# Optimization experiments

Hardware: AMD Instinct MI355X
Metric: run time of the kernel (lower is better)

## Reference

```python
import jax, jax.numpy as jnp
import numpy as np

N, E, D, LM, NF, M = 512, 16384, 1280, 1024, 256, 64

def setup_inputs() -> dict:
    key = jax.random.key(0)
    ks = jax.random.split(key, 10)
    lm_embedding = jax.random.normal(ks[0], (1, N + 2, LM), jnp.float32)
    node_feat = jax.random.normal(ks[1], (N, NF), jnp.float32)
    edge_feat = jax.random.uniform(ks[2], (E, 1), jnp.float32)
    src = jax.random.randint(ks[3], (E,), 0, N)
    dst = jax.random.randint(ks[4], (E,), 0, N)
    mask_index = jax.random.randint(ks[5], (M,), 0, N)
    W_g = jax.random.normal(ks[6], (D, D), jnp.float32) / np.sqrt(D).astype(np.float32)
    b_g = jnp.zeros((D,), jnp.float32)
    W_d = jax.random.normal(ks[7], (D, 1), jnp.float32) / np.sqrt(D).astype(np.float32)
    b_d = jnp.zeros((1,), jnp.float32)
    W_m = jax.random.normal(ks[8], (D, 2), jnp.float32) / np.sqrt(D).astype(np.float32)
    b_m = jnp.zeros((2,), jnp.float32)
    return {"lm_embedding": lm_embedding, "node_feat": node_feat, "edge_feat": edge_feat,
            "src": src, "dst": dst, "mask_index": mask_index,
            "W_g": W_g, "b_g": b_g, "W_d": W_d, "b_d": b_d, "W_m": W_m, "b_m": b_m}

def reference(lm_embedding, node_feat, edge_feat, src, dst, mask_index,
              W_g, b_g, W_d, b_d, W_m, b_m):
    # concat LM embedding (strip BOS/EOS) with structural features -> (N, D)
    h = jnp.concatenate([lm_embedding[0, 1:-1, :], node_feat], axis=1)
    # GINConv('max'): messages = h[src] * edge_weight, max-reduce onto dst
    msg = h[src] * edge_feat                                   # (E, D)
    neigh = jax.ops.segment_max(msg, dst, num_segments=h.shape[0])
    neigh = jnp.where(jnp.isneginf(neigh), 0.0, neigh)         # isolated nodes -> 0 (DGL semantics)
    rst = (h + neigh) @ W_g + b_g                              # (1+eps)*h + neigh, eps=0, then Linear
    node_output = rst + h                                      # residual
    # dis_pred[i, j] = sigmoid(W_d . (h_j - h_i) + b_d); collapse to per-node projection
    p = (node_output @ W_d)[:, 0]                              # (N,)
    dis_pred = jax.nn.sigmoid(p[None, :] - p[:, None] + b_d[0])[..., None]  # (N, N, 1)
    mask_pred = jnp.tanh(node_output[mask_index] @ W_m + b_m)  # (M, 2)
    return (dis_pred, mask_pred)
```

## Files before the change

### kernel.cpp

```cpp
#include <hip/hip_runtime.h>
#include <float.h>
#include <math.h>

#define N 512
#define E 16384
#define D 1280
#define LMDIM 1024
#define NFDIM 256
#define M 64
#define MAXDEG 512

__device__ __forceinline__ float4 h_vec4(const float* __restrict__ lm,
                                         const float* __restrict__ nf,
                                         int i, int t) {
  return (t < 256) ? *(const float4*)&lm[(size_t)(i + 1) * LMDIM + t * 4]
                   : *(const float4*)&nf[(size_t)i * NFDIM + (t - 256) * 4];
}

__device__ __forceinline__ void reduce3_320(float* s0, float* s1, float* s2,
                                            int t, float v0, float v1, float v2) {
  s0[t] = v0; s1[t] = v1; s2[t] = v2;
  __syncthreads();
  if (t < 64) {
    s0[t] += s0[t + 256];
    s1[t] += s1[t + 256];
    s2[t] += s2[t + 256];
  }
  __syncthreads();
  for (int off = 128; off > 0; off >>= 1) {
    if (t < off) {
      s0[t] += s0[t + off];
      s1[t] += s1[t + off];
      s2[t] += s2[t + off];
    }
    __syncthreads();
  }
}

__global__ __launch_bounds__(320) void wproj_kernel(const float* __restrict__ Wg,
                                                    const float* __restrict__ Wd,
                                                    const float* __restrict__ Wm,
                                                    const float* __restrict__ bg,
                                                    float* __restrict__ wd2,
                                                    float* __restrict__ wm2,
                                                    float* __restrict__ consts) {
  __shared__ float s0[320], s1[320], s2[320];
  int b = blockIdx.x;
  int t = threadIdx.x;
  const float* row = (b < D) ? &Wg[(size_t)b * D] : bg;
  float4 wv = *(const float4*)&row[t * 4];
  float4 vd = *(const float4*)&Wd[t * 4];
  float d0 = wv.x * vd.x + wv.y * vd.y + wv.z * vd.z + wv.w * vd.w;
  float4 m01 = *(const float4*)&Wm[t * 8];
  float4 m23 = *(const float4*)&Wm[t * 8 + 4];
  float d1 = wv.x * m01.x + wv.y * m01.z + wv.z * m23.x + wv.w * m23.z;
  float d2 = wv.x * m01.y + wv.y * m01.w + wv.z * m23.y + wv.w * m23.w;
  reduce3_320(s0, s1, s2, t, d0, d1, d2);
  if (t == 0) {
    if (b < D) {
      wd2[b] = s0[0];
      wm2[b * 2 + 0] = s1[0];
      wm2[b * 2 + 1] = s2[0];
    } else {
      consts[0] = s0[0];
      consts[1] = s1[0];
      consts[2] = s2[0];
    }
  }
}

__global__ __launch_bounds__(320) void neighp_kernel(const float* __restrict__ lm,
                                                     const float* __restrict__ nf,
                                                     const float* __restrict__ ew,
                                                     const int* __restrict__ src,
                                                     const int* __restrict__ dst,
                                                     const int* __restrict__ mask_index,
                                                     const float* __restrict__ Wd,
                                                     const float* __restrict__ Wm,
                                                     const float* __restrict__ bm,
                                                     const float* __restrict__ wd2,
                                                     const float* __restrict__ wm2,
                                                     const float* __restrict__ consts,
                                                     float* __restrict__ p,
                                                     float* __restrict__ out) {
  __shared__ int   s_e[MAXDEG];
  __shared__ int   s_src[MAXDEG];
  __shared__ float s_w[MAXDEG];
  __shared__ int   s_cnt;
  __shared__ float s0[320], s1[320], s2[320];

  int n = blockIdx.x;
  int t = threadIdx.x;
  if (t == 0) s_cnt = 0;
  __syncthreads();

  const int4* dst4 = (const int4*)dst;
  for (int i = t; i < E / 4; i += 320) {
    int4 d4 = dst4[i];
    if (d4.x == n) { int pos = atomicAdd(&s_cnt, 1); if (pos < MAXDEG) s_e[pos] = 4 * i + 0; }
    if (d4.y == n) { int pos = atomicAdd(&s_cnt, 1); if (pos < MAXDEG) s_e[pos] = 4 * i + 1; }
    if (d4.z == n) { int pos = atomicAdd(&s_cnt, 1); if (pos < MAXDEG) s_e[pos] = 4 * i + 2; }
    if (d4.w == n) { int pos = atomicAdd(&s_cnt, 1); if (pos < MAXDEG) s_e[pos] = 4 * i + 3; }
  }
  __syncthreads();
  int cnt = min(s_cnt, MAXDEG);
  for (int i = t; i < cnt; i += 320) {
    int e = s_e[i];
    s_src[i] = src[e];
    s_w[i] = ew[e];
  }
  __syncthreads();
  float4 m = make_float4(-FLT_MAX, -FLT_MAX, -FLT_MAX, -FLT_MAX);
  int i = 0;
  for (; i + 8 <= cnt; i += 8) {
    float4 v[8];
    float wgt[8];
#pragma unroll
    for (int j = 0; j < 8; ++j) {
      int s = s_src[i + j];
      wgt[j] = s_w[i + j];
      v[j] = h_vec4(lm, nf, s, t);
    }
#pragma unroll
    for (int j = 0; j < 8; ++j) {
      m.x = fmaxf(m.x, v[j].x * wgt[j]);
      m.y = fmaxf(m.y, v[j].y * wgt[j]);
      m.z = fmaxf(m.z, v[j].z * wgt[j]);
      m.w = fmaxf(m.w, v[j].w * wgt[j]);
    }
  }
  for (; i < cnt; ++i) {
    int s = s_src[i];
    float wgt = s_w[i];
    float4 v = h_vec4(lm, nf, s, t);
    m.x = fmaxf(m.x, v.x * wgt);
    m.y = fmaxf(m.y, v.y * wgt);
    m.z = fmaxf(m.z, v.z * wgt);
    m.w = fmaxf(m.w, v.w * wgt);
  }
  bool has = (cnt > 0);
  float4 hv = h_vec4(lm, nf, n, t);
  float4 a;
  a.x = hv.x + (has ? m.x : 0.0f);
  a.y = hv.y + (has ? m.y : 0.0f);
  a.z = hv.z + (has ? m.z : 0.0f);
  a.w = hv.w + (has ? m.w : 0.0f);

  float4 w2 = *(const float4*)&wd2[t * 4];
  float4 vd = *(const float4*)&Wd[t * 4];
  float pd = a.x * w2.x + a.y * w2.y + a.z * w2.z + a.w * w2.w
           + hv.x * vd.x + hv.y * vd.y + hv.z * vd.z + hv.w * vd.w;
  float4 q01 = *(const float4*)&wm2[t * 8];
  float4 q23 = *(const float4*)&wm2[t * 8 + 4];
  float4 m01 = *(const float4*)&Wm[t * 8];
  float4 m23 = *(const float4*)&Wm[t * 8 + 4];
  float a0 = a.x * q01.x + a.y * q01.z + a.z * q23.x + a.w * q23.z
           + hv.x * m01.x + hv.y * m01.z + hv.z * m23.x + hv.w * m23.z;
  float a1 = a.x * q01.y + a.y * q01.w + a.z * q23.y + a.w * q23.w
           + hv.x * m01.y + hv.y * m01.w + hv.z * m23.y + hv.w * m23.w;

  reduce3_320(s0, s1, s2, t, pd, a0, a1);
  if (t == 0) p[n] = s0[0] + consts[0];
  if (t < M) {
    if (mask_index[t] == n) {
      out[(size_t)N * N + t * 2 + 0] = tanhf(s1[0] + consts[1] + bm[0]);
      out[(size_t)N * N + t * 2 + 1] = tanhf(s2[0] + consts[2] + bm[1]);
    }
  }
}

__global__ __launch_bounds__(256) void dis_kernel(const float* __restrict__ p,
                                                  const float* __restrict__ bd,
                                                  float* __restrict__ out) {
  int b = blockIdx.x;
  int t = threadIdx.x;
  int i = b * 2 + (t >> 7);
  int j4 = (t & 127) * 4;
  float pi = p[i];
  float bias = bd[0];
  float4 pj = *(const float4*)&p[j4];
  float4 o;
  o.x = 1.0f / (1.0f + __expf(-(pj.x - pi + bias)));
  o.y = 1.0f / (1.0f + __expf(-(pj.y - pi + bias)));
  o.z = 1.0f / (1.0f + __expf(-(pj.z - pi + bias)));
  o.w = 1.0f / (1.0f + __expf(-(pj.w - pi + bias)));
  *(float4*)&out[(size_t)i * N + j4] = o;
}


extern "C" void kernel_launch(void* const* d_in, const int* in_sizes, int n_in,
                              void* d_out, int out_size, void* d_ws, size_t ws_size,
                              hipStream_t stream) {
  const float* lm = (const float*)d_in[0];
  const float* nf = (const float*)d_in[1];
  const float* ew = (const float*)d_in[2];
  const int* src = (const int*)d_in[3];
  const int* dst = (const int*)d_in[4];
  const int* mask_index = (const int*)d_in[5];
  const float* Wg = (const float*)d_in[6];
  const float* bg = (const float*)d_in[7];
  const float* Wd = (const float*)d_in[8];
  const float* bd = (const float*)d_in[9];
  const float* Wm = (const float*)d_in[10];
  const float* bm = (const float*)d_in[11];
  float* out = (float*)d_out;
  char* w = (char*)d_ws;

  float* wd2    = (float*)(w);
  float* wm2    = (float*)(w + 5120);
  float* consts = (float*)(w + 15360);
  float* p      = (float*)(w + 15488);

  wproj_kernel<<<D + 1, 320, 0, stream>>>(Wg, Wd, Wm, bg, wd2, wm2, consts);
  neighp_kernel<<<N, 320, 0, stream>>>(lm, nf, ew, src, dst, mask_index,
                                       Wd, Wm, bm, wd2, wm2, consts, p, out);
  dis_kernel<<<N / 2, 256, 0, stream>>>(p, bd, out);
}
```

Measured before the change: 98.56 us.

## Fuse projection, aggregation and sigmoid stages into one cooperative kernel

Merges the three launches (weight projection, neighbor max aggregation with projection, pairwise sigmoid) into a single cooperative kernel with two grid-wide syncs. Each block's wavefronts compute weight-projection rows before the neighbor gather, so that work overlaps with the aggregation. Block reductions now use wavefront shuffles instead of shared-memory trees. The aim is to remove launch gaps and sync overhead, at the cost of grid-sync latency and a cooperative launch that requires all 512 blocks to be resident.

```diff
diff --git a/kernel.cpp b/kernel.cpp
--- a/kernel.cpp
+++ b/kernel.cpp
@@ -1,6 +1,9 @@
 #include <hip/hip_runtime.h>
+#include <hip/hip_cooperative_groups.h>
 #include <float.h>
 #include <math.h>
+
+namespace cg = cooperative_groups;
 
 #define N 512
 #define E 16384
@@ -17,81 +20,65 @@
                    : *(const float4*)&nf[(size_t)i * NFDIM + (t - 256) * 4];
 }
 
-__device__ __forceinline__ void reduce3_320(float* s0, float* s1, float* s2,
-                                            int t, float v0, float v1, float v2) {
-  s0[t] = v0; s1[t] = v1; s2[t] = v2;
-  __syncthreads();
-  if (t < 64) {
-    s0[t] += s0[t + 256];
-    s1[t] += s1[t + 256];
-    s2[t] += s2[t + 256];
-  }
-  __syncthreads();
-  for (int off = 128; off > 0; off >>= 1) {
-    if (t < off) {
-      s0[t] += s0[t + off];
-      s1[t] += s1[t + off];
-      s2[t] += s2[t + off];
-    }
-    __syncthreads();
-  }
-}
-
-__global__ __launch_bounds__(320) void wproj_kernel(const float* __restrict__ Wg,
-                                                    const float* __restrict__ Wd,
-                                                    const float* __restrict__ Wm,
-                                                    const float* __restrict__ bg,
-                                                    float* __restrict__ wd2,
-                                                    float* __restrict__ wm2,
-                                                    float* __restrict__ consts) {
-  __shared__ float s0[320], s1[320], s2[320];
-  int b = blockIdx.x;
-  int t = threadIdx.x;
-  const float* row = (b < D) ? &Wg[(size_t)b * D] : bg;
-  float4 wv = *(const float4*)&row[t * 4];
-  float4 vd = *(const float4*)&Wd[t * 4];
-  float d0 = wv.x * vd.x + wv.y * vd.y + wv.z * vd.z + wv.w * vd.w;
-  float4 m01 = *(const float4*)&Wm[t * 8];
-  float4 m23 = *(const float4*)&Wm[t * 8 + 4];
-  float d1 = wv.x * m01.x + wv.y * m01.z + wv.z * m23.x + wv.w * m23.z;
-  float d2 = wv.x * m01.y + wv.y * m01.w + wv.z * m23.y + wv.w * m23.w;
-  reduce3_320(s0, s1, s2, t, d0, d1, d2);
-  if (t == 0) {
-    if (b < D) {
-      wd2[b] = s0[0];
-      wm2[b * 2 + 0] = s1[0];
-      wm2[b * 2 + 1] = s2[0];
-    } else {
-      consts[0] = s0[0];
-      consts[1] = s1[0];
-      consts[2] = s2[0];
-    }
-  }
-}
-
-__global__ __launch_bounds__(320) void neighp_kernel(const float* __restrict__ lm,
-                                                     const float* __restrict__ nf,
-                                                     const float* __restrict__ ew,
-                                                     const int* __restrict__ src,
-                                                     const int* __restrict__ dst,
-                                                     const int* __restrict__ mask_index,
-                                                     const float* __restrict__ Wd,
-                                                     const float* __restrict__ Wm,
-                                                     const float* __restrict__ bm,
-                                                     const float* __restrict__ wd2,
-                                                     const float* __restrict__ wm2,
-                                                     const float* __restrict__ consts,
-                                                     float* __restrict__ p,
-                                                     float* __restrict__ out) {
+__device__ __forceinline__ float wred(float v) {
+#pragma unroll
+  for (int off = 32; off > 0; off >>= 1) v += __shfl_xor(v, off, 64);
+  return v;
+}
+
+__global__ __launch_bounds__(320) void fused_kernel(
+    const float* __restrict__ lm, const float* __restrict__ nf,
+    const float* __restrict__ ew, const int* __restrict__ src,
+    const int* __restrict__ dst, const int* __restrict__ mask_index,
+    const float* __restrict__ Wg, const float* __restrict__ Wd,
+    const float* __restrict__ Wm, const float* __restrict__ bg,
+    const float* __restrict__ bd, const float* __restrict__ bm,
+    float* __restrict__ wd2, float* __restrict__ wm2,
+    float* __restrict__ consts, float* __restrict__ p,
+    float* __restrict__ out) {
   __shared__ int   s_e[MAXDEG];
   __shared__ int   s_src[MAXDEG];
   __shared__ float s_w[MAXDEG];
   __shared__ int   s_cnt;
-  __shared__ float s0[320], s1[320], s2[320];
-
-  int n = blockIdx.x;
-  int t = threadIdx.x;
+  __shared__ float r0s[5], r1s[5], r2s[5];
+  __shared__ float s_m1, s_m2;
+
+  cg::grid_group grid = cg::this_grid();
+  const int n = blockIdx.x;
+  const int t = threadIdx.x;
+  const int wid = t >> 6;
+  const int lane = t & 63;
+
   if (t == 0) s_cnt = 0;
+
+  {
+    int r = wid * N + n;
+    if (r <= D) {
+      const float* row = (r < D) ? &Wg[(size_t)r * D] : bg;
+      float d0 = 0.f, d1 = 0.f, d2 = 0.f;
+#pragma unroll
+      for (int k = 0; k < 5; ++k) {
+        int u = lane + 64 * k;
+        float4 wv = *(const float4*)&row[u * 4];
+        float4 vd = *(const float4*)&Wd[u * 4];
+        d0 += wv.x * vd.x + wv.y * vd.y + wv.z * vd.z + wv.w * vd.w;
+        float4 m01 = *(const float4*)&Wm[u * 8];
+        float4 m23 = *(const float4*)&Wm[u * 8 + 4];
+        d1 += wv.x * m01.x + wv.y * m01.z + wv.z * m23.x + wv.w * m23.z;
+        d2 += wv.x * m01.y + wv.y * m01.w + wv.z * m23.y + wv.w * m23.w;
+      }
+      d0 = wred(d0); d1 = wred(d1); d2 = wred(d2);
+      if (lane == 0) {
+        if (r < D) {
+          wd2[r] = d0; wm2[2 * r] = d1; wm2[2 * r + 1] = d2;
+        } else {
+          consts[0] = d0; consts[1] = d1; consts[2] = d2;
+        }
+        __threadfence();
+      }
+    }
+  }
+
   __syncthreads();
 
   const int4* dst4 = (const int4*)dst;
@@ -110,6 +97,7 @@
     s_w[i] = ew[e];
   }
   __syncthreads();
+
   float4 m = make_float4(-FLT_MAX, -FLT_MAX, -FLT_MAX, -FLT_MAX);
   int i = 0;
   for (; i + 8 <= cnt; i += 8) {
@@ -145,6 +133,8 @@
   a.y = hv.y + (has ? m.y : 0.0f);
   a.z = hv.z + (has ? m.z : 0.0f);
   a.w = hv.w + (has ? m.w : 0.0f);
+
+  grid.sync();
 
   float4 w2 = *(const float4*)&wd2[t * 4];
   float4 vd = *(const float4*)&Wd[t * 4];
@@ -159,32 +149,37 @@
   float a1 = a.x * q01.y + a.y * q01.w + a.z * q23.y + a.w * q23.w
            + hv.x * m01.y + hv.y * m01.w + hv.z * m23.y + hv.w * m23.w;
 
-  reduce3_320(s0, s1, s2, t, pd, a0, a1);
-  if (t == 0) p[n] = s0[0] + consts[0];
-  if (t < M) {
-    if (mask_index[t] == n) {
-      out[(size_t)N * N + t * 2 + 0] = tanhf(s1[0] + consts[1] + bm[0]);
-      out[(size_t)N * N + t * 2 + 1] = tanhf(s2[0] + consts[2] + bm[1]);
-    }
-  }
-}
-
-__global__ __launch_bounds__(256) void dis_kernel(const float* __restrict__ p,
-                                                  const float* __restrict__ bd,
-                                                  float* __restrict__ out) {
-  int b = blockIdx.x;
-  int t = threadIdx.x;
-  int i = b * 2 + (t >> 7);
-  int j4 = (t & 127) * 4;
-  float pi = p[i];
-  float bias = bd[0];
-  float4 pj = *(const float4*)&p[j4];
-  float4 o;
-  o.x = 1.0f / (1.0f + __expf(-(pj.x - pi + bias)));
-  o.y = 1.0f / (1.0f + __expf(-(pj.y - pi + bias)));
-  o.z = 1.0f / (1.0f + __expf(-(pj.z - pi + bias)));
-  o.w = 1.0f / (1.0f + __expf(-(pj.w - pi + bias)));
-  *(float4*)&out[(size_t)i * N + j4] = o;
+  pd = wred(pd); a0 = wred(a0); a1 = wred(a1);
+  if (lane == 0) { r0s[wid] = pd; r1s[wid] = a0; r2s[wid] = a1; }
+  __syncthreads();
+  if (t == 0) {
+    float sp = r0s[0] + r0s[1] + r0s[2] + r0s[3] + r0s[4];
+    float s1 = r1s[0] + r1s[1] + r1s[2] + r1s[3] + r1s[4];
+    float s2 = r2s[0] + r2s[1] + r2s[2] + r2s[3] + r2s[4];
+    p[n] = sp + consts[0];
+    s_m1 = s1 + consts[1];
+    s_m2 = s2 + consts[2];
+    __threadfence();
+  }
+  __syncthreads();
+  if (t < M && mask_index[t] == n) {
+    out[(size_t)N * N + t * 2 + 0] = tanhf(s_m1 + bm[0]);
+    out[(size_t)N * N + t * 2 + 1] = tanhf(s_m2 + bm[1]);
+  }
+
+  grid.sync();
+
+  if (t < 128) {
+    float pi = p[n];
+    float bias = bd[0];
+    float4 pj = *(const float4*)&p[t * 4];
+    float4 o;
+    o.x = 1.0f / (1.0f + __expf(-(pj.x - pi + bias)));
+    o.y = 1.0f / (1.0f + __expf(-(pj.y - pi + bias)));
+    o.z = 1.0f / (1.0f + __expf(-(pj.z - pi + bias)));
+    o.w = 1.0f / (1.0f + __expf(-(pj.w - pi + bias)));
+    *(float4*)&out[(size_t)n * N + t * 4] = o;
+  }
 }
 
 
@@ -211,8 +206,12 @@
   float* consts = (float*)(w + 15360);
   float* p      = (float*)(w + 15488);
 
-  wproj_kernel<<<D + 1, 320, 0, stream>>>(Wg, Wd, Wm, bg, wd2, wm2, consts);
-  neighp_kernel<<<N, 320, 0, stream>>>(lm, nf, ew, src, dst, mask_index,
-                                       Wd, Wm, bm, wd2, wm2, consts, p, out);
-  dis_kernel<<<N / 2, 256, 0, stream>>>(p, bd, out);
-}
+  void* args[17] = {
+    (void*)&lm, (void*)&nf, (void*)&ew, (void*)&src, (void*)&dst,
+    (void*)&mask_index, (void*)&Wg, (void*)&Wd, (void*)&Wm, (void*)&bg,
+    (void*)&bd, (void*)&bm, (void*)&wd2, (void*)&wm2, (void*)&consts,
+    (void*)&p, (void*)&out
+  };
+  (void)hipLaunchCooperativeKernel((void*)fused_kernel, dim3(N), dim3(320),
+                                   args, 0, stream);
+}
```

Result: slower. 268.8 us (+172.7%).
